# Performance work log

Measured on AMD Instinct MI355X. Metric: run time of the kernel, lower is better.

The kernel has to match this reference:

```python
import jax, jax.numpy as jnp
import numpy as np
from jax import lax

DIM = 128
HEADS = 2
SR = 4
HID = 512  # 4 * DIM
DROPKEY_P = 0.1


def _ln(x, g, b, eps=1e-5):
    m = jnp.mean(x, axis=-1, keepdims=True)
    v = jnp.var(x, axis=-1, keepdims=True)
    return (x - m) / jnp.sqrt(v + eps) * g + b


def _block(x, H, W, params, key):
    (n1g, n1b, qw, kvw, srw, srb, sng, snb, pw, pb,
     n2g, n2b, f1w, f1b, dww, dwb, f2w, f2b) = params
    B, N, C = x.shape
    dh = C // HEADS
    scale = dh ** -0.5
    # --- spatial-reduction attention ---
    h = _ln(x, n1g, n1b)
    q = (h @ qw.T).reshape(B, N, HEADS, dh).transpose(0, 2, 1, 3)  # [B,h,N,dh]
    xi = h.transpose(0, 2, 1).reshape(B, C, H, W)
    xs = lax.conv_general_dilated(xi, srw, (SR, SR), 'VALID',
                                  dimension_numbers=('NCHW', 'OIHW', 'NCHW'))
    xs = xs + srb[None, :, None, None]
    Np = (H // SR) * (W // SR)
    xs = xs.reshape(B, C, Np).transpose(0, 2, 1)  # [B,N',C]
    xs = _ln(xs, sng, snb)
    kv = (xs @ kvw.T).reshape(B, Np, 2, HEADS, dh).transpose(2, 0, 3, 1, 4)
    k, v = kv[0], kv[1]  # [B,h,N',dh]
    attn = jnp.einsum('bhnd,bhmd->bhnm', q, k) * scale
    # dropkey: bernoulli(p) mask pushed to -1e12 before softmax (always applied)
    mask = jax.random.bernoulli(key, DROPKEY_P, attn.shape)
    attn = attn + mask.astype(attn.dtype) * (-1e12)
    attn = jax.nn.softmax(attn, axis=-1)
    o = jnp.einsum('bhnm,bhmd->bhnd', attn, v).transpose(0, 2, 1, 3).reshape(B, N, C)
    x = x + o @ pw.T + pb
    # --- MLP with depthwise conv ---
    h2 = _ln(x, n2g, n2b)
    h2 = h2 @ f1w.T + f1b  # [B,N,HID]
    hi = h2.transpose(0, 2, 1).reshape(B, HID, H, W)
    hi = lax.conv_general_dilated(hi, dww, (1, 1), 'SAME',
                                  feature_group_count=HID,
                                  dimension_numbers=('NCHW', 'OIHW', 'NCHW'))
    hi = hi + dwb[None, :, None, None]
    h2 = hi.reshape(B, HID, N).transpose(0, 2, 1)
    h2 = jax.nn.gelu(h2, approximate=False)
    x = x + h2 @ f2w.T + f2b
    return x


def setup_inputs() -> dict:
    key = jax.random.key(0)
    ks = jax.random.split(key, 10)
    p = {}
    p['x'] = jax.random.normal(ks[0], (16, 2 * DIM, 56, 56), jnp.float32)
    p['concat_w'] = jax.random.normal(ks[1], (DIM, 2 * DIM), jnp.float32) * 0.02
    p['concat_b'] = jnp.zeros((DIM,), jnp.float32)
    # two Blocks -> leading dim 2 on all per-block params
    p['norm1_g'] = jnp.ones((2, DIM), jnp.float32)
    p['norm1_b'] = jnp.zeros((2, DIM), jnp.float32)
    p['q_w'] = jax.random.normal(ks[2], (2, DIM, DIM), jnp.float32) * 0.02
    p['kv_w'] = jax.random.normal(ks[3], (2, 2 * DIM, DIM), jnp.float32) * 0.02
    p['sr_w'] = jax.random.normal(ks[4], (2, DIM, DIM, SR, SR), jnp.float32) * 0.03
    p['sr_b'] = jnp.zeros((2, DIM), jnp.float32)
    p['srn_g'] = jnp.ones((2, DIM), jnp.float32)
    p['srn_b'] = jnp.zeros((2, DIM), jnp.float32)
    p['proj_w'] = jax.random.normal(ks[5], (2, DIM, DIM), jnp.float32) * 0.02
    p['proj_b'] = jnp.zeros((2, DIM), jnp.float32)
    p['norm2_g'] = jnp.ones((2, DIM), jnp.float32)
    p['norm2_b'] = jnp.zeros((2, DIM), jnp.float32)
    p['fc1_w'] = jax.random.normal(ks[6], (2, HID, DIM), jnp.float32) * 0.02
    p['fc1_b'] = jnp.zeros((2, HID), jnp.float32)
    p['dw_w'] = jax.random.normal(ks[7], (2, HID, 1, 3, 3), jnp.float32) * 0.1
    p['dw_b'] = jnp.zeros((2, HID), jnp.float32)
    p['fc2_w'] = jax.random.normal(ks[8], (2, DIM, HID), jnp.float32) * 0.02
    p['fc2_b'] = jnp.zeros((2, DIM), jnp.float32)
    return p


def reference(x, concat_w, concat_b, norm1_g, norm1_b, q_w, kv_w, sr_w, sr_b,
              srn_g, srn_b, proj_w, proj_b, norm2_g, norm2_b, fc1_w, fc1_b,
              dw_w, dw_b, fc2_w, fc2_b):
    b, c, h, w = x.shape
    xs = x.transpose(0, 2, 3, 1).reshape(b, h * w, c)
    xs = xs @ concat_w.T + concat_b  # [B,N,DIM]
    mkey = jax.random.key(42)
    stacked = (norm1_g, norm1_b, q_w, kv_w, sr_w, sr_b, srn_g, srn_b, proj_w,
               proj_b, norm2_g, norm2_b, fc1_w, fc1_b, dw_w, dw_b, fc2_w, fc2_b)
    for i in range(2):
        params_i = tuple(p[i] for p in stacked)
        xs = _block(xs, h, w, params_i, jax.random.fold_in(mkey, i))
    return xs.reshape(b, h, w, DIM).transpose(0, 3, 1, 2)
```

## Files before the change

### kernel.cpp

```cpp
#include <hip/hip_runtime.h>
#include <stdint.h>

typedef __attribute__((ext_vector_type(8))) short short8;
typedef __attribute__((ext_vector_type(4))) float f32x4;
typedef __attribute__((ext_vector_type(2))) float f32x2;
typedef unsigned short u16;
typedef uint32_t u32;
typedef unsigned long long u64;

__host__ __device__ static inline void threefry(u32 k0, u32 k1, u32 x0, u32 x1,
                                                u32* o0, u32* o1) {
  u32 ks2 = k0 ^ k1 ^ 0x1BD11BDAu;
  x0 += k0; x1 += k1;
#define TF_RR(r) { x0 += x1; x1 = (x1 << (r)) | (x1 >> (32 - (r))); x1 ^= x0; }
  TF_RR(13) TF_RR(15) TF_RR(26) TF_RR(6)
  x0 += k1;  x1 += ks2 + 1u;
  TF_RR(17) TF_RR(29) TF_RR(16) TF_RR(24)
  x0 += ks2; x1 += k0 + 2u;
  TF_RR(13) TF_RR(15) TF_RR(26) TF_RR(6)
  x0 += k0;  x1 += k1 + 3u;
  TF_RR(17) TF_RR(29) TF_RR(16) TF_RR(24)
  x0 += k1;  x1 += ks2 + 4u;
  TF_RR(13) TF_RR(15) TF_RR(26) TF_RR(6)
  x0 += ks2; x1 += k0 + 5u;
#undef TF_RR
  *o0 = x0; *o1 = x1;
}

__device__ static inline float bf2f(u16 u) {
  union { u32 i; float f; } v; v.i = ((u32)u) << 16; return v.f;
}
__device__ static inline u16 f2bf(float f) {
  union { float f; u32 i; } v; v.f = f;
  u32 x = v.i;
  return (u16)((x + 0x7FFFu + ((x >> 16) & 1u)) >> 16);
}
__device__ static inline float lo_bf(u32 w) {
  union { u32 i; float f; } v; v.i = w << 16; return v.f;
}
__device__ static inline float hi_bf(u32 w) {
  union { u32 i; float f; } v; v.i = w & 0xFFFF0000u; return v.f;
}
__device__ static inline bool is_f32(const u32* ng) { return ng[0] == 0x3F800000u; }

typedef const uint32_t __attribute__((address_space(1)))* gas_ptr;
typedef uint32_t __attribute__((address_space(3)))* las_ptr;
__device__ static inline void gld16(const u16* g, u16* l) {
  __builtin_amdgcn_global_load_lds((gas_ptr)(const void*)g, (las_ptr)(void*)l, 16, 0, 0);
}

#define MASK_HALF 9834496u

__global__ __launch_bounds__(256) void mask_gen2(u32* __restrict__ MSK2, u32 k0, u32 k1) {
  int t = blockIdx.x * 256 + threadIdx.x;
  if (t >= 351232) return;
  int w = t % 7;
  int rowbh = t / 7;
  u32 base = (u32)rowbh * 196u + (u32)w * 32u;
  int kmax = 196 - w * 32;
  if (kmax > 32) kmax = 32;
  u32 bits0 = 0, bits1 = 0;
  for (int j = 0; j < kmax; j++) {
    u32 o0, o1;
    threefry(k0, k1, base + (u32)j, base + (u32)j + MASK_HALF, &o0, &o1);
    union { u32 u; float f; } u0, u1;
    u0.u = (o0 >> 9) | 0x3F800000u;
    u1.u = (o1 >> 9) | 0x3F800000u;
    if (u0.f - 1.0f < 0.1f) bits0 |= (1u << j);
    if (u1.f - 1.0f < 0.1f) bits1 |= (1u << j);
  }
  MSK2[(size_t)rowbh * 7 + w] = bits0;
  MSK2[(size_t)(rowbh + 50176) * 7 + w] = bits1;
}

struct PtrTab { const void* p[20]; };
#define ARENA_N 963968
#define VT_WORDS 229376

__global__ __launch_bounds__(256) void convert_params(PtrTab tab, u16* __restrict__ arena,
                                                      u32* __restrict__ VT) {
  const int cum[21] = {0, 32768, 32896, 33152, 33408, 66176, 131712, 656000, 656256,
                       656512, 656768, 689536, 689792, 690048, 690304, 821376, 822400,
                       831616, 832640, 963712, 963968};
  int idx = blockIdx.x * 256 + threadIdx.x;
  if (idx >= ARENA_N) {
    int v = idx - ARENA_N;
    if (v < VT_WORDS) VT[v] = 0;
    return;
  }
  bool f32m = (((const u32*)tab.p[2])[0] == 0x3F800000u);
  int t = 0;
  while (idx >= cum[t + 1]) t++;
  int local = idx - cum[t];
  if (t == 16) {
    int blk = local / 4608, r = local - blk * 4608;
    int wi = r >> 9, c = r & 511;
    local = blk * 4608 + c * 9 + wi;
  } else if (t == 6) {
    int blk = local / 262144, r = local - blk * 262144;
    int o = r >> 11, kp = r & 2047;
    int ij = kp >> 7, c = kp & 127;
    local = blk * 262144 + o * 2048 + c * 16 + ij;
  }
  u16 v;
  if (f32m) v = f2bf(((const float*)tab.p[t])[local]);
  else      v = ((const u16*)tab.p[t])[local];
  arena[idx] = v;
}

__global__ __launch_bounds__(256) void transpose_in(const void* __restrict__ Xin,
                                                    const u32* __restrict__ ng,
                                                    u16* __restrict__ Xt) {
  bool f32m = is_f32(ng);
  __shared__ u16 tile[64][65];
  int n0 = blockIdx.x * 64, c0 = blockIdx.y * 64, b = blockIdx.z;
  int tx = threadIdx.x & 63, ty = threadIdx.x >> 6;
  if (f32m) {
    const float* src = (const float*)Xin + (size_t)b * 256 * 3136;
#pragma unroll
    for (int i = 0; i < 16; i++) {
      int cl = i * 4 + ty;
      tile[cl][tx] = f2bf(src[(size_t)(c0 + cl) * 3136 + n0 + tx]);
    }
  } else {
    const u16* src = (const u16*)Xin + (size_t)b * 256 * 3136;
#pragma unroll
    for (int i = 0; i < 16; i++) {
      int cl = i * 4 + ty;
      tile[cl][tx] = src[(size_t)(c0 + cl) * 3136 + n0 + tx];
    }
  }
  __syncthreads();
  u16* dst = Xt + (size_t)b * 3136 * 256;
#pragma unroll
  for (int i = 0; i < 16; i++) {
    int nl = i * 4 + ty;
    dst[(size_t)(n0 + nl) * 256 + c0 + tx] = tile[tx][nl];
  }
}

__global__ __launch_bounds__(256) void transpose_out(const u16* __restrict__ X,
                                                     const u32* __restrict__ ng,
                                                     void* __restrict__ Out) {
  bool f32m = is_f32(ng);
  __shared__ u16 tile[64][65];
  int n0 = blockIdx.x * 64, d0 = blockIdx.y * 64, b = blockIdx.z;
  int tx = threadIdx.x & 63, ty = threadIdx.x >> 6;
#pragma unroll
  for (int i = 0; i < 16; i++) {
    int nl = i * 4 + ty;
    tile[nl][tx] = X[((size_t)b * 3136 + n0 + nl) * 128 + d0 + tx];
  }
  __syncthreads();
#pragma unroll
  for (int i = 0; i < 16; i++) {
    int dl = i * 4 + ty;
    size_t o = ((size_t)b * 128 + d0 + dl) * 3136 + n0 + tx;
    if (f32m) ((float*)Out)[o] = bf2f(tile[tx][dl]);
    else      ((u16*)Out)[o]   = tile[tx][dl];
  }
}

__global__ __launch_bounds__(256) __attribute__((amdgpu_waves_per_eu(2, 4)))
void gemm_tiled(const u16* __restrict__ A,
                const u16* __restrict__ W,
                const u16* __restrict__ bias,
                u16* __restrict__ outB,
                u16* __restrict__ outVT,
                int M, int N, int K, int mode) {
  __shared__ __align__(16) u16 smem[17408];
  u16* AlsP = smem;
  u16* BlsP = smem + 8192;
  int n0 = blockIdx.y * 128, m0 = blockIdx.x * 128;
  int tid = threadIdx.x, wv = tid >> 6, lane = tid & 63;
  int wr = wv >> 1, wc = wv & 1;
  int l15 = lane & 15, hh = lane >> 4, lk = hh * 8;
  int srow = wv * 32 + (lane >> 2);
  int scol = (lane & 3) * 8;

  f32x4 acc[4][4];
#pragma unroll
  for (int m = 0; m < 4; m++)
#pragma unroll
    for (int n = 0; n < 4; n++) acc[m][n] = (f32x4){0.f, 0.f, 0.f, 0.f};

#define STAGE(buf, k0)                                                          \
  {                                                                             \
    _Pragma("unroll") for (int i = 0; i < 2; i++) {                             \
      int ar = m0 + srow + i * 16;                                              \
      if (ar >= M) ar = M - 1;                                                  \
      gld16(A + (size_t)ar * K + (k0) + scol,                                   \
            AlsP + (buf) * 4096 + (wv * 32 + i * 16) * 32);                     \
      int br = n0 + srow + i * 16;                                              \
      gld16(W + (size_t)br * K + (k0) + scol,                                   \
            BlsP + (buf) * 4096 + (wv * 32 + i * 16) * 32);                     \
    }                                                                           \
  }

  int nt = K >> 5;
  STAGE(0, 0);
  int cur = 0;
  for (int t = 0; t < nt; t++) {
    __syncthreads();
    if (t + 1 < nt) STAGE(cur ^ 1, (t + 1) * 32);
    short8 af[4], bf[4];
#pragma unroll
    for (int m = 0; m < 4; m++)
      af[m] = *(const short8*)(AlsP + cur * 4096 + (wr * 64 + m * 16 + l15) * 32 + lk);
#pragma unroll
    for (int n = 0; n < 4; n++)
      bf[n] = *(const short8*)(BlsP + cur * 4096 + (wc * 64 + n * 16 + l15) * 32 + lk);
#pragma unroll
    for (int m = 0; m < 4; m++)
#pragma unroll
      for (int n = 0; n < 4; n++)
        acc[m][n] = __builtin_amdgcn_mfma_f32_16x16x32_bf16(af[m], bf[n], acc[m][n], 0, 0, 0);
    cur ^= 1;
  }
#undef STAGE

  if (mode == 0) {
    __syncthreads();
#pragma unroll
    for (int n = 0; n < 4; n++) {
      int col = wc * 64 + n * 16 + l15;
      float bv = bias ? bf2f(bias[n0 + col]) : 0.0f;
#pragma unroll
      for (int m = 0; m < 4; m++) {
        int rbase = wr * 64 + m * 16 + hh * 4;
#pragma unroll
        for (int r = 0; r < 4; r++)
          smem[(rbase + r) * 136 + col] = f2bf(acc[m][n][r] + bv);
      }
    }
    __syncthreads();
#pragma unroll
    for (int p = 0; p < 8; p++) {
      int row = p * 16 + (tid >> 4);
      int colb = (tid & 15) * 8;
      int grow = m0 + row;
      if (grow < M) {
        short8 v = *(const short8*)&smem[row * 136 + colb];
        *(short8*)(outB + (size_t)grow * N + n0 + colb) = v;
      }
    }
    return;
  }

#pragma unroll
  for (int n = 0; n < 4; n++) {
    int col = n0 + wc * 64 + n * 16 + l15;
#pragma unroll
    for (int m = 0; m < 4; m++) {
      int rbase = m0 + wr * 64 + m * 16 + hh * 4;
#pragma unroll
      for (int r = 0; r < 4; r++) {
        int row = rbase + r;
        if (row < M) {
          float v = acc[m][n][r];
          if (col < 128) outB[(size_t)row * 128 + col] = f2bf(v);
          else {
            int hd = (col - 128) >> 6, d = (col - 128) & 63;
            int b = row / 196, key = row - b * 196;
            outVT[(size_t)((b * 2 + hd) * 64 + d) * 224 + key] = f2bf(v);
          }
        }
      }
    }
  }
}

__global__ __launch_bounds__(256) __attribute__((amdgpu_waves_per_eu(2, 4)))
void gemm_n128(const u16* __restrict__ A,
               const u16* __restrict__ W,
               const u16* __restrict__ bias,
               u16* __restrict__ Xb,
               u16* __restrict__ outB,
               const u16* __restrict__ lnG,
               const u16* __restrict__ lnB,
               u16* __restrict__ outH,
               const u16* __restrict__ qW,
               u16* __restrict__ outQ,
               int M, int K, int mode) {
  __shared__ __align__(16) u16 smem[12288];
  __shared__ float sumsA[64][4];
  __shared__ float sumsB[64][4];
  u16* Als = smem;
  u16* Bls = smem + 4096;
  int m0 = blockIdx.y * 64;
  int tid = threadIdx.x, wv = tid >> 6, lane = tid & 63;
  int l15 = lane & 15, hq = lane >> 4, lk = hq * 8;
  int scol = (lane & 3) * 8;

  f32x4 acc[4][2];
#pragma unroll
  for (int m = 0; m < 4; m++)
#pragma unroll
    for (int n = 0; n < 2; n++) acc[m][n] = (f32x4){0.f, 0.f, 0.f, 0.f};

#define STAGE(buf, k0)                                                          \
  {                                                                             \
    int ar = m0 + wv * 16 + (lane >> 2);                                        \
    if (ar >= M) ar = M - 1;                                                    \
    gld16(A + (size_t)ar * K + (k0) + scol, Als + (buf) * 2048 + wv * 512);     \
    _Pragma("unroll") for (int i = 0; i < 2; i++) {                             \
      int br = wv * 32 + i * 16 + (lane >> 2);                                  \
      gld16(W + (size_t)br * K + (k0) + scol,                                   \
            Bls + (buf) * 4096 + wv * 1024 + i * 512);                          \
    }                                                                           \
  }

  int nt = K >> 5;
  STAGE(0, 0);
  int cur = 0;
  for (int t = 0; t < nt; t++) {
    __syncthreads();
    if (t + 1 < nt) STAGE(cur ^ 1, (t + 1) * 32);
    short8 af[4], bf[2];
#pragma unroll
    for (int m = 0; m < 4; m++)
      af[m] = *(const short8*)(Als + cur * 2048 + (m * 16 + l15) * 32 + lk);
#pragma unroll
    for (int n = 0; n < 2; n++)
      bf[n] = *(const short8*)(Bls + cur * 4096 + (wv * 32 + n * 16 + l15) * 32 + lk);
#pragma unroll
    for (int m = 0; m < 4; m++)
#pragma unroll
      for (int n = 0; n < 2; n++)
        acc[m][n] = __builtin_amdgcn_mfma_f32_16x16x32_bf16(af[m], bf[n], acc[m][n], 0, 0, 0);
    cur ^= 1;
  }
#undef STAGE

  if (mode == 2) {
#pragma unroll
    for (int n = 0; n < 2; n++) {
      int col = wv * 32 + n * 16 + l15;
      float bv = bias ? bf2f(bias[col]) : 0.0f;
#pragma unroll
      for (int m = 0; m < 4; m++) {
        int rbase = m0 + m * 16 + hq * 4;
#pragma unroll
        for (int r = 0; r < 4; r++) {
          size_t idx = (size_t)(rbase + r) * 128 + col;
          Xb[idx] = f2bf(bf2f(Xb[idx]) + acc[m][n][r] + bv);
        }
      }
    }
    return;
  }

  if (mode >= 4) {
#pragma unroll
    for (int n = 0; n < 2; n++) {
      int col = wv * 32 + n * 16 + l15;
      float bv = bias ? bf2f(bias[col]) : 0.0f;
#pragma unroll
      for (int m = 0; m < 4; m++) {
        int rbase = m0 + m * 16 + hq * 4;
#pragma unroll
        for (int r = 0; r < 4; r++) {
          size_t idx = (size_t)(rbase + r) * 128 + col;
          float v = acc[m][n][r] + bv;
          if (mode == 5) v += bf2f(Xb[idx]);
          acc[m][n][r] = v;
          Xb[idx] = f2bf(v);
        }
      }
    }
#pragma unroll
    for (int m = 0; m < 4; m++) {
#pragma unroll
      for (int r = 0; r < 4; r++) {
        float a = acc[m][0][r] + acc[m][1][r];
        float b = acc[m][0][r] * acc[m][0][r] + acc[m][1][r] * acc[m][1][r];
#pragma unroll
        for (int d = 1; d < 16; d <<= 1) {
          a += __shfl_xor(a, d);
          b += __shfl_xor(b, d);
        }
        if (l15 == 0) {
          int lrow = m * 16 + hq * 4 + r;
          sumsA[lrow][wv] = a;
          sumsB[lrow][wv] = b;
        }
      }
    }
    __syncthreads();
#pragma unroll
    for (int m = 0; m < 4; m++) {
#pragma unroll
      for (int r = 0; r < 4; r++) {
        int lrow = m * 16 + hq * 4 + r;
        float t1 = sumsA[lrow][0] + sumsA[lrow][1] + sumsA[lrow][2] + sumsA[lrow][3];
        float t2 = sumsB[lrow][0] + sumsB[lrow][1] + sumsB[lrow][2] + sumsB[lrow][3];
        float mean = t1 * 0.0078125f;
        float var = t2 * 0.0078125f - mean * mean;
        float inv = 1.0f / sqrtf(var + 1e-5f);
#pragma unroll
        for (int n = 0; n < 2; n++) {
          int col = wv * 32 + n * 16 + l15;
          float g = bf2f(lnG[col]), bb2 = bf2f(lnB[col]);
          smem[lrow * 136 + col] = f2bf((acc[m][n][r] - mean) * inv * g + bb2);
        }
      }
    }
    __syncthreads();
#pragma unroll
    for (int p = 0; p < 4; p++) {
      int row = p * 16 + (tid >> 4);
      int colb = (tid & 15) * 8;
      short8 v = *(const short8*)&smem[row * 136 + colb];
      *(short8*)(outH + (size_t)(m0 + row) * 128 + colb) = v;
    }

    if (qW) {
#pragma unroll
      for (int m = 0; m < 4; m++)
#pragma unroll
        for (int n = 0; n < 2; n++) acc[m][n] = (f32x4){0.f, 0.f, 0.f, 0.f};
#pragma unroll
      for (int kc = 0; kc < 4; kc++) {
        short8 af[4], bf[2];
#pragma unroll
        for (int m = 0; m < 4; m++)
          af[m] = *(const short8*)&smem[(m * 16 + l15) * 136 + kc * 32 + lk];
#pragma unroll
        for (int n = 0; n < 2; n++)
          bf[n] = *(const short8*)(qW + (size_t)(wv * 32 + n * 16 + l15) * 128 +
                                   kc * 32 + lk);
#pragma unroll
        for (int m = 0; m < 4; m++)
#pragma unroll
          for (int n = 0; n < 2; n++)
            acc[m][n] =
                __builtin_amdgcn_mfma_f32_16x16x32_bf16(af[m], bf[n], acc[m][n], 0, 0, 0);
      }
      __syncthreads();
#pragma unroll
      for (int n = 0; n < 2; n++) {
        int col = wv * 32 + n * 16 + l15;
#pragma unroll
        for (int m = 0; m < 4; m++) {
          int rbase = m * 16 + hq * 4;
#pragma unroll
          for (int r = 0; r < 4; r++)
            smem[(rbase + r) * 136 + col] = f2bf(acc[m][n][r]);
        }
      }
      __syncthreads();
#pragma unroll
      for (int p = 0; p < 4; p++) {
        int row = p * 16 + (tid >> 4);
        int colb = (tid & 15) * 8;
        short8 v = *(const short8*)&smem[row * 136 + colb];
        *(short8*)(outQ + (size_t)(m0 + row) * 128 + colb) = v;
      }
    }
    return;
  }

  __syncthreads();
#pragma unroll
  for (int n = 0; n < 2; n++) {
    int col = wv * 32 + n * 16 + l15;
    float bv = bias ? bf2f(bias[col]) : 0.0f;
#pragma unroll
    for (int m = 0; m < 4; m++) {
      int rbase = m * 16 + hq * 4;
#pragma unroll
      for (int r = 0; r < 4; r++)
        smem[(rbase + r) * 136 + col] = f2bf(acc[m][n][r] + bv);
    }
  }
  __syncthreads();
#pragma unroll
  for (int p = 0; p < 4; p++) {
    int row = p * 16 + (tid >> 4);
    int colb = (tid & 15) * 8;
    short8 v = *(const short8*)&smem[row * 136 + colb];
    *(short8*)(outB + (size_t)(m0 + row) * 128 + colb) = v;
  }
}

__global__ __launch_bounds__(256) void gemm_splitk(const u16* __restrict__ Hsrc,
                                                   const u16* __restrict__ W,
                                                   float* __restrict__ PS,
                                                   int M, int N, int K) {
  __shared__ __align__(16) u16 Als[2][4096];
  __shared__ __align__(16) u16 Bls[2][4096];
  int n0 = blockIdx.x * 128, m0 = blockIdx.y * 128, ks = blockIdx.z;
  int tid = threadIdx.x, wv = tid >> 6, lane = tid & 63;
  int wr = wv >> 1, wc = wv & 1;
  int l15 = lane & 15, lk = (lane >> 4) * 8;
  int srow = wv * 32 + (lane >> 2);
  int scol = (lane & 3) * 8;

  f32x4 acc[4][4];
#pragma unroll
  for (int m = 0; m < 4; m++)
#pragma unroll
    for (int n = 0; n < 4; n++) acc[m][n] = (f32x4){0.f, 0.f, 0.f, 0.f};

#define STAGE(buf, k0)                                                          \
  {                                                                             \
    _Pragma("unroll") for (int i = 0; i < 2; i++) {                             \
      int ar = m0 + srow + i * 16;                                              \
      if (ar >= M) ar = M - 1;                                                  \
      int bb = ar / 196, pp = ar - bb * 196;                                    \
      int ph = pp / 14, pw = pp - ph * 14;                                      \
      int kk = (k0) + scol;                                                     \
      int ij = kk >> 7, c = kk & 127;                                           \
      int n2 = (4 * ph + (ij >> 2)) * 56 + 4 * pw + (ij & 3);                   \
      gld16(Hsrc + ((size_t)(bb * 3136 + n2)) * 128 + c,                        \
            &Als[buf][(wv * 32 + i * 16) * 32]);                                \
      int br = n0 + srow + i * 16;                                              \
      gld16(W + (size_t)br * K + (k0) + scol,                                   \
            &Bls[buf][(wv * 32 + i * 16) * 32]);                                \
    }                                                                           \
  }

  int kbeg = ks * 128;
  STAGE(0, kbeg);
  int cur = 0;
  for (int t = 0; t < 4; t++) {
    __syncthreads();
    if (t + 1 < 4) STAGE(cur ^ 1, kbeg + (t + 1) * 32);
    short8 af[4], bf[4];
#pragma unroll
    for (int m = 0; m < 4; m++)
      af[m] = *(const short8*)(&Als[cur][(wr * 64 + m * 16 + l15) * 32 + lk]);
#pragma unroll
    for (int n = 0; n < 4; n++)
      bf[n] = *(const short8*)(&Bls[cur][(wc * 64 + n * 16 + l15) * 32 + lk]);
#pragma unroll
    for (int m = 0; m < 4; m++)
#pragma unroll
      for (int n = 0; n < 4; n++)
        acc[m][n] = __builtin_amdgcn_mfma_f32_16x16x32_bf16(af[m], bf[n], acc[m][n], 0, 0, 0);
    cur ^= 1;
  }
#undef STAGE

  float* myPS = PS + (size_t)ks * M * N;
#pragma unroll
  for (int n = 0; n < 4; n++) {
    int col = n0 + wc * 64 + n * 16 + l15;
#pragma unroll
    for (int m = 0; m < 4; m++) {
      int rbase = m0 + wr * 64 + m * 16 + (lane >> 4) * 4;
#pragma unroll
      for (int r = 0; r < 4; r++) {
        int row = rbase + r;
        if (row < M) myPS[(size_t)row * N + col] = acc[m][n][r];
      }
    }
  }
}

__global__ __launch_bounds__(256) void splitk_reduce_ln(const float* __restrict__ PS,
                                                        const u16* __restrict__ bias,
                                                        const u16* __restrict__ G,
                                                        const u16* __restrict__ Bi,
                                                        u16* __restrict__ XSN) {
  __shared__ float red[4][2];
  int tid = threadIdx.x;
  int row = blockIdx.x * 2 + (tid >> 7);
  int col = tid & 127;
  int t = row * 128 + col;
  float s = bf2f(bias[col]);
#pragma unroll
  for (int k = 0; k < 16; k++) s += PS[(size_t)k * 401408 + t];
  float s1 = s, s2 = s * s;
#pragma unroll
  for (int d = 1; d < 64; d <<= 1) {
    s1 += __shfl_xor(s1, d);
    s2 += __shfl_xor(s2, d);
  }
  int wv = tid >> 6;
  if ((tid & 63) == 0) { red[wv][0] = s1; red[wv][1] = s2; }
  __syncthreads();
  int other = wv ^ 1;
  float t1 = red[wv][0] + red[other][0];
  float t2 = red[wv][1] + red[other][1];
  float mean = t1 * 0.0078125f;
  float var = t2 * 0.0078125f - mean * mean;
  float inv = 1.0f / sqrtf(var + 1e-5f);
  XSN[t] = f2bf((s - mean) * inv * bf2f(G[col]) + bf2f(Bi[col]));
}

__global__ __launch_bounds__(256) __attribute__((amdgpu_waves_per_eu(2, 4)))
void attn_kernel(const u16* __restrict__ Q,
                 const u16* __restrict__ Kb,
                 const u16* __restrict__ VT,
                 const u32* __restrict__ M2,
                 u16* __restrict__ O) {
  __shared__ __align__(16) u16 smA[14848];
  int t = blockIdx.x;
  int tp = (t & 7) * 196 + (t >> 3);
  int bh = tp / 49, qt = tp - bh * 49;
  int b = bh >> 1, hd = bh & 1;
  int q0 = qt * 64;
  int tid = threadIdx.x;

  int wv = tid >> 6, lane = tid & 63;
  int l15 = lane & 15, h = lane >> 4, lk = h * 8;

  {
    const u16* ksrc = Kb + (size_t)b * 196 * 128 + hd * 64;
    for (int idx = tid; idx < 1568; idx += 256) {
      int row = idx >> 3, ch = idx & 7;
      short8 v = *(const short8*)(ksrc + (size_t)row * 128 + ch * 8);
      *(short8*)&smA[row * 68 + ch * 8] = v;
    }
  }

  const u16* qp = Q + ((size_t)(b * 3136 + q0 + wv * 16 + l15) * 128) + hd * 64 + lk;
  short8 aq0 = *(const short8*)(qp);
  short8 aq1 = *(const short8*)(qp + 32);
  int rowg = q0 + wv * 16 + h * 4;

  u32 mwv[4][7];
  const u32* mwbase = M2 + (size_t)(bh * 3136 + rowg) * 7;
#pragma unroll
  for (int r = 0; r < 4; r++)
#pragma unroll
    for (int w = 0; w < 7; w++) mwv[r][w] = mwbase[r * 7 + w];

  __syncthreads();

  float sarr[13][4];
#pragma unroll
  for (int cc = 0; cc < 13; cc++) {
    int key = cc * 16 + l15;
    int keyc = key > 195 ? 195 : key;
    short8 kb0 = *(const short8*)&smA[keyc * 68 + lk];
    short8 kb1 = *(const short8*)&smA[keyc * 68 + 32 + lk];
    f32x4 s = {0.f, 0.f, 0.f, 0.f};
    s = __builtin_amdgcn_mfma_f32_16x16x32_bf16(aq0, kb0, s, 0, 0, 0);
    s = __builtin_amdgcn_mfma_f32_16x16x32_bf16(aq1, kb1, s, 0, 0, 0);
#pragma unroll
    for (int r = 0; r < 4; r++) sarr[cc][r] = s[r] * 0.125f;
  }

#pragma unroll
  for (int cc = 0; cc < 13; cc++) {
    bool keyok = (cc * 16 + l15) < 196;
    int pos = (cc & 3) * 16 + l15;
#pragma unroll
    for (int r = 0; r < 4; r++) {
      u64 mm = (cc < 4) ? ((u64)mwv[r][0] | ((u64)mwv[r][1] << 32))
             : (cc < 8) ? ((u64)mwv[r][2] | ((u64)mwv[r][3] << 32))
             : (cc < 12) ? ((u64)mwv[r][4] | ((u64)mwv[r][5] << 32))
                         : ((u64)mwv[r][6]);
      bool drop = (mm >> pos) & 1ull;
      if (!keyok || drop) sarr[cc][r] = -3.0e38f;
    }
  }

  float mx[4] = {sarr[0][0], sarr[0][1], sarr[0][2], sarr[0][3]};
#pragma unroll
  for (int cc = 1; cc < 13; cc++)
#pragma unroll
    for (int r = 0; r < 4; r++) mx[r] = fmaxf(mx[r], sarr[cc][r]);
#pragma unroll
  for (int d = 1; d < 16; d <<= 1)
#pragma unroll
    for (int r = 0; r < 4; r++) mx[r] = fmaxf(mx[r], __shfl_xor(mx[r], d));
  float sm[4] = {0.f, 0.f, 0.f, 0.f};
#pragma unroll
  for (int cc = 0; cc < 13; cc++)
#pragma unroll
    for (int r = 0; r < 4; r++) {
      float p = __expf(sarr[cc][r] - mx[r]);
      sarr[cc][r] = p;
      sm[r] += p;
    }
#pragma unroll
  for (int d = 1; d < 16; d <<= 1)
#pragma unroll
    for (int r = 0; r < 4; r++) sm[r] += __shfl_xor(sm[r], d);
  float inv[4];
#pragma unroll
  for (int r = 0; r < 4; r++)
    asm("v_rcp_f32 %0, %1" : "=v"(inv[r]) : "v"(sm[r]));

  __syncthreads();

#pragma unroll
  for (int cc = 0; cc < 13; cc++)
#pragma unroll
    for (int r = 0; r < 4; r++)
      smA[(wv * 16 + h * 4 + r) * 232 + cc * 16 + l15] = f2bf(sarr[cc][r] * inv[r]);
#pragma unroll
  for (int rj = 0; rj < 4; rj++) smA[(wv * 16 + l15) * 232 + 208 + h * 4 + rj] = 0;

  const u16* vbase = VT + (size_t)(bh * 64) * 224;
  short8 vw[4];
#pragma unroll
  for (int i = 0; i < 4; i++) {
    vw[i] = *(const short8*)(vbase + (size_t)(0 * 16 + l15) * 224 + i * 32 + lk);
  }
#pragma unroll
  for (int dc = 0; dc < 4; dc++) {
    f32x4 oa = {0.f, 0.f, 0.f, 0.f};
#pragma unroll
    for (int kc = 0; kc < 7; kc++) {
      int i = dc * 7 + kc;
      short8 bv = vw[i & 3];
      if (i + 4 < 28) {
        int i2 = i + 4;
        int dc2 = i2 / 7, kc2 = i2 - dc2 * 7;
        vw[i & 3] =
            *(const short8*)(vbase + (size_t)(dc2 * 16 + l15) * 224 + kc2 * 32 + lk);
      }
      short8 a = *(const short8*)&smA[(wv * 16 + l15) * 232 + kc * 32 + lk];
      oa = __builtin_amdgcn_mfma_f32_16x16x32_bf16(a, bv, oa, 0, 0, 0);
    }
#pragma unroll
    for (int r = 0; r < 4; r++) {
      O[((size_t)(b * 3136 + rowg + r) * 128) + hd * 64 + dc * 16 + l15] = f2bf(oa[r]);
    }
  }
}

__global__ __launch_bounds__(256) __attribute__((amdgpu_waves_per_eu(2, 4)))
void dwconv_gelu(const u16* __restrict__ H2,
                 const u16* __restrict__ Wdw,
                 const u16* __restrict__ Bdw,
                 u16* __restrict__ Out) {
  int tid = threadIdx.x;
  int wv = tid >> 6, lane = tid & 63;
  int sb = blockIdx.x;
  int wg = (sb & 7) * 392 + (sb >> 3);
  int strip = wg * 4 + wv;
  int bb = strip / 784;
  int s = strip - bb * 784;
  int y = s / 14, x0 = (s - y * 14) * 4;
  int c0 = lane * 8;

  f32x2 wf[9][4];
#pragma unroll
  for (int t9 = 0; t9 < 9; t9++) {
    short8 w8 = *(const short8*)(Wdw + t9 * 512 + c0);
#pragma unroll
    for (int p = 0; p < 4; p++) {
      u32 w = ((const u32*)&w8)[p];
      wf[t9][p] = (f32x2){lo_bf(w), hi_bf(w)};
    }
  }
  f32x2 acc[4][4];
  {
    short8 b8 = *(const short8*)(Bdw + c0);
#pragma unroll
    for (int p = 0; p < 4; p++) {
      u32 w = ((const u32*)&b8)[p];
      f32x2 bv = {lo_bf(w), hi_bf(w)};
#pragma unroll
      for (int q = 0; q < 4; q++) acc[q][p] = bv;
    }
  }

  const u16* base = H2 + ((size_t)bb * 3136) * 512 + c0;
#pragma unroll
  for (int di = -1; di <= 1; di++) {
    int y2 = y + di;
    if (y2 < 0 || y2 >= 56) continue;
    const u16* rowp = base + (size_t)(y2 * 56) * 512;
#pragma unroll
    for (int j = 0; j < 6; j++) {
      int c = x0 - 1 + j;
      if (c < 0 || c > 55) continue;
      short8 h8 = *(const short8*)(rowp + (size_t)c * 512);
      f32x2 hf[4];
#pragma unroll
      for (int p = 0; p < 4; p++) {
        u32 w = ((const u32*)&h8)[p];
        hf[p] = (f32x2){lo_bf(w), hi_bf(w)};
      }
      int wrow = (di + 1) * 3;
#pragma unroll
      for (int q = 0; q < 4; q++) {
        int dx = j - 1 - q;
        if (dx < -1 || dx > 1) continue;
#pragma unroll
        for (int p = 0; p < 4; p++) acc[q][p] += hf[p] * wf[wrow + dx + 1][p];
      }
    }
  }

  size_t obase = ((size_t)(bb * 3136 + y * 56 + x0)) * 512 + c0;
#pragma unroll
  for (int q = 0; q < 4; q++) {
    short8 ov;
#pragma unroll
    for (int p = 0; p < 4; p++) {
      float g2[2];
#pragma unroll
      for (int e = 0; e < 2; e++) {
        float v = acc[q][p][e];
        float tt = v * v;
        float yn = v * (-2.3022088f - 0.1029434f * tt);
        float ex;
        asm("v_exp_f32 %0, %1" : "=v"(ex) : "v"(yn));
        float den = 1.0f + ex;
        float sg;
        asm("v_rcp_f32 %0, %1" : "=v"(sg) : "v"(den));
        g2[e] = v * sg;
      }
      u32 pk;
      asm("v_cvt_pk_bf16_f32 %0, %1, %2" : "=v"(pk) : "v"(g2[0]), "v"(g2[1]));
      ((u32*)&ov)[p] = pk;
    }
    *(short8*)(Out + obase + (size_t)q * 512) = ov;
  }
}

__global__ __launch_bounds__(256) void fill_sentinel(void* __restrict__ Out,
                                                     const u32* __restrict__ ng, int n) {
  bool f32m = is_f32(ng);
  int t = blockIdx.x * 256 + threadIdx.x;
  if (t >= n) return;
  if (f32m) ((float*)Out)[t] = 12345.0f;
  else      ((u16*)Out)[t]   = f2bf(12345.0f);
}

extern "C" void kernel_launch(void* const* d_in, const int* in_sizes, int n_in,
                              void* d_out, int out_size, void* d_ws, size_t ws_size,
                              hipStream_t stream) {
  (void)in_sizes; (void)n_in;
  const u32* ng = (const u32*)d_in[3];

  const size_t o_X   = 0;
  const size_t o_H   = 25690112;
  const size_t o_R   = o_H + 12845056;
  const size_t o_Q   = o_R;
  const size_t o_O   = o_R + 12845056;
  const size_t o_Xt  = o_R + 25690112;
  const size_t o_H2C = o_R;
  const size_t o_H2  = o_R + 51380224;
  const size_t o_XSN = o_H2 + 51380224;
  const size_t o_KB  = o_XSN + 802816;
  const size_t o_VT  = o_KB + 802816;
  const size_t o_M2  = o_VT + 917504;
  const size_t o_AR  = o_M2 + 2809856;
  const size_t NEED  = o_AR + (size_t)ARENA_N * 2;

  if (ws_size < NEED) {
    fill_sentinel<<<(out_size + 255) / 256, 256, 0, stream>>>(d_out, ng, out_size);
    return;
  }

  char* ws = (char*)d_ws;
  u16* Xb   = (u16*)(ws + o_X);
  u16* H    = (u16*)(ws + o_H);
  u16* Qb   = (u16*)(ws + o_Q);
  u16* Ob   = (u16*)(ws + o_O);
  u16* Xt   = (u16*)(ws + o_Xt);
  u16* H2C  = (u16*)(ws + o_H2C);
  u16* H2   = (u16*)(ws + o_H2);
  float* PS = (float*)(ws + o_H2);
  u16* XSN  = (u16*)(ws + o_XSN);
  u16* Kb   = (u16*)(ws + o_KB);
  u16* VT   = (u16*)(ws + o_VT);
  u32* MSK2 = (u32*)(ws + o_M2);
  u16* AR   = (u16*)(ws + o_AR);

  PtrTab tab;
  for (int j = 0; j < 20; j++) tab.p[j] = d_in[j + 1];
  convert_params<<<(ARENA_N + VT_WORDS + 255) / 256, 256, 0, stream>>>(tab, AR, (u32*)VT);

  u16* ACW  = AR + 0;      u16* ACB  = AR + 32768;
  u16* AN1G = AR + 32896;  u16* AN1B = AR + 33152;
  u16* AQW  = AR + 33408;  u16* AKVW = AR + 66176;
  u16* ASRW = AR + 131712; u16* ASRB = AR + 656000;
  u16* ASNG = AR + 656256; u16* ASNB = AR + 656512;
  u16* APW  = AR + 656768; u16* APB  = AR + 689536;
  u16* AN2G = AR + 689792; u16* AN2B = AR + 690048;
  u16* AF1W = AR + 690304; u16* AF1B = AR + 821376;
  u16* ADWW = AR + 822400; u16* ADWB = AR + 831616;
  u16* AF2W = AR + 832640; u16* AF2B = AR + 963712;

  transpose_in<<<dim3(49, 4, 16), 256, 0, stream>>>(d_in[0], ng, Xt);
  gemm_n128<<<dim3(1, 784), 256, 0, stream>>>(Xt, ACW, ACB, Xb, nullptr,
                                              AN1G, AN1B, H, AQW, Qb,
                                              50176, 256, 4);

  for (int i = 0; i < 2; i++) {
    u32 fk0, fk1;
    threefry(0u, 42u, 0u, (u32)i, &fk0, &fk1);

    gemm_splitk<<<dim3(1, 25, 16), 256, 0, stream>>>(H, ASRW + i * 262144, PS,
                                                     3136, 128, 2048);
    mask_gen2<<<1372, 256, 0, stream>>>(MSK2, fk0, fk1);
    splitk_reduce_ln<<<1568, 256, 0, stream>>>(PS, ASRB + i * 128,
                                               ASNG + i * 128, ASNB + i * 128, XSN);

    gemm_tiled<<<dim3(25, 2), 256, 0, stream>>>(XSN, AKVW + i * 32768, nullptr,
                                                Kb, VT, 3136, 256, 128, 3);
    attn_kernel<<<1568, 256, 0, stream>>>(Qb, Kb, VT, MSK2, Ob);
    gemm_n128<<<dim3(1, 784), 256, 0, stream>>>(Ob, APW + i * 16384, APB + i * 128,
                                                Xb, nullptr,
                                                AN2G + i * 128, AN2B + i * 128, H,
                                                nullptr, nullptr, 50176, 128, 5);
    gemm_tiled<<<dim3(392, 4), 256, 0, stream>>>(H, AF1W + i * 65536, AF1B + i * 512,
                                                 H2, nullptr,
                                                 50176, 512, 128, 0);
    dwconv_gelu<<<3136, 256, 0, stream>>>(H2, ADWW + i * 4608, ADWB + i * 512, H2C);
    if (i == 0) {
      gemm_n128<<<dim3(1, 784), 256, 0, stream>>>(H2C, AF2W, AF2B, Xb, nullptr,
                                                  AN1G + 128, AN1B + 128, H,
                                                  AQW + 16384, Qb, 50176, 512, 5);
    } else {
      gemm_n128<<<dim3(1, 784), 256, 0, stream>>>(H2C, AF2W + 65536, AF2B + 128,
                                                  Xb, nullptr, nullptr, nullptr, nullptr,
                                                  nullptr, nullptr, 50176, 512, 2);
    }
  }

  transpose_out<<<dim3(49, 2, 16), 256, 0, stream>>>(Xb, ng, d_out);
}
```

Before: 410.0 us.

## Restructure gemm_n128 so each wave owns 16 full rows, dropping LDS staging

Each wave now computes a 16x128 output tile, with A and W fragments loaded straight from global memory instead of being staged through double-buffered shared memory. LayerNorm row statistics are then reduced with shuffles inside the wave, so the cross-wave shared-memory sums and the block barriers go away. The fused Q projection also runs per wave on the wave's own LDS slice. In exchange W is re-read from global/L2 by every wave with no LDS reuse, the mode<4 plain-output path (outB) is removed, and the M bounds clamp is dropped.

```diff
diff --git a/kernel.cpp b/kernel.cpp
--- a/kernel.cpp
+++ b/kernel.cpp
@@ -282,204 +282,115 @@
                const u16* __restrict__ qW,
                u16* __restrict__ outQ,
                int M, int K, int mode) {
-  __shared__ __align__(16) u16 smem[12288];
-  __shared__ float sumsA[64][4];
-  __shared__ float sumsB[64][4];
-  u16* Als = smem;
-  u16* Bls = smem + 4096;
-  int m0 = blockIdx.y * 64;
+  (void)outB; (void)M;
+  __shared__ __align__(16) u16 smem[8704];
   int tid = threadIdx.x, wv = tid >> 6, lane = tid & 63;
-  int l15 = lane & 15, hq = lane >> 4, lk = hq * 8;
-  int scol = (lane & 3) * 8;
-
-  f32x4 acc[4][2];
-#pragma unroll
-  for (int m = 0; m < 4; m++)
-#pragma unroll
-    for (int n = 0; n < 2; n++) acc[m][n] = (f32x4){0.f, 0.f, 0.f, 0.f};
-
-#define STAGE(buf, k0)                                                          \
-  {                                                                             \
-    int ar = m0 + wv * 16 + (lane >> 2);                                        \
-    if (ar >= M) ar = M - 1;                                                    \
-    gld16(A + (size_t)ar * K + (k0) + scol, Als + (buf) * 2048 + wv * 512);     \
-    _Pragma("unroll") for (int i = 0; i < 2; i++) {                             \
-      int br = wv * 32 + i * 16 + (lane >> 2);                                  \
-      gld16(W + (size_t)br * K + (k0) + scol,                                   \
-            Bls + (buf) * 4096 + wv * 1024 + i * 512);                          \
-    }                                                                           \
-  }
-
+  int l15 = lane & 15, h = lane >> 4, lk = h * 8;
+  int mw = blockIdx.y * 64 + wv * 16;
+  u16* ws = smem + wv * 2176;
+
+  f32x4 acc[8];
+#pragma unroll
+  for (int n = 0; n < 8; n++) acc[n] = (f32x4){0.f, 0.f, 0.f, 0.f};
+
+  const u16* arow = A + (size_t)(mw + l15) * K + lk;
   int nt = K >> 5;
-  STAGE(0, 0);
-  int cur = 0;
   for (int t = 0; t < nt; t++) {
-    __syncthreads();
-    if (t + 1 < nt) STAGE(cur ^ 1, (t + 1) * 32);
-    short8 af[4], bf[2];
-#pragma unroll
-    for (int m = 0; m < 4; m++)
-      af[m] = *(const short8*)(Als + cur * 2048 + (m * 16 + l15) * 32 + lk);
-#pragma unroll
-    for (int n = 0; n < 2; n++)
-      bf[n] = *(const short8*)(Bls + cur * 4096 + (wv * 32 + n * 16 + l15) * 32 + lk);
-#pragma unroll
-    for (int m = 0; m < 4; m++)
-#pragma unroll
-      for (int n = 0; n < 2; n++)
-        acc[m][n] = __builtin_amdgcn_mfma_f32_16x16x32_bf16(af[m], bf[n], acc[m][n], 0, 0, 0);
-    cur ^= 1;
-  }
-#undef STAGE
+    short8 af = *(const short8*)(arow + t * 32);
+    short8 bf[8];
+#pragma unroll
+    for (int n = 0; n < 8; n++)
+      bf[n] = *(const short8*)(W + (size_t)(n * 16 + l15) * K + t * 32 + lk);
+#pragma unroll
+    for (int n = 0; n < 8; n++)
+      acc[n] = __builtin_amdgcn_mfma_f32_16x16x32_bf16(af, bf[n], acc[n], 0, 0, 0);
+  }
 
   if (mode == 2) {
 #pragma unroll
-    for (int n = 0; n < 2; n++) {
-      int col = wv * 32 + n * 16 + l15;
+    for (int n = 0; n < 8; n++) {
+      int col = n * 16 + l15;
       float bv = bias ? bf2f(bias[col]) : 0.0f;
 #pragma unroll
-      for (int m = 0; m < 4; m++) {
-        int rbase = m0 + m * 16 + hq * 4;
-#pragma unroll
-        for (int r = 0; r < 4; r++) {
-          size_t idx = (size_t)(rbase + r) * 128 + col;
-          Xb[idx] = f2bf(bf2f(Xb[idx]) + acc[m][n][r] + bv);
-        }
+      for (int r = 0; r < 4; r++) {
+        size_t idx = (size_t)(mw + h * 4 + r) * 128 + col;
+        Xb[idx] = f2bf(bf2f(Xb[idx]) + acc[n][r] + bv);
       }
     }
     return;
   }
 
-  if (mode >= 4) {
-#pragma unroll
-    for (int n = 0; n < 2; n++) {
-      int col = wv * 32 + n * 16 + l15;
-      float bv = bias ? bf2f(bias[col]) : 0.0f;
-#pragma unroll
-      for (int m = 0; m < 4; m++) {
-        int rbase = m0 + m * 16 + hq * 4;
-#pragma unroll
-        for (int r = 0; r < 4; r++) {
-          size_t idx = (size_t)(rbase + r) * 128 + col;
-          float v = acc[m][n][r] + bv;
-          if (mode == 5) v += bf2f(Xb[idx]);
-          acc[m][n][r] = v;
-          Xb[idx] = f2bf(v);
-        }
-      }
-    }
-#pragma unroll
-    for (int m = 0; m < 4; m++) {
-#pragma unroll
-      for (int r = 0; r < 4; r++) {
-        float a = acc[m][0][r] + acc[m][1][r];
-        float b = acc[m][0][r] * acc[m][0][r] + acc[m][1][r] * acc[m][1][r];
-#pragma unroll
-        for (int d = 1; d < 16; d <<= 1) {
-          a += __shfl_xor(a, d);
-          b += __shfl_xor(b, d);
-        }
-        if (l15 == 0) {
-          int lrow = m * 16 + hq * 4 + r;
-          sumsA[lrow][wv] = a;
-          sumsB[lrow][wv] = b;
-        }
-      }
-    }
-    __syncthreads();
-#pragma unroll
-    for (int m = 0; m < 4; m++) {
-#pragma unroll
-      for (int r = 0; r < 4; r++) {
-        int lrow = m * 16 + hq * 4 + r;
-        float t1 = sumsA[lrow][0] + sumsA[lrow][1] + sumsA[lrow][2] + sumsA[lrow][3];
-        float t2 = sumsB[lrow][0] + sumsB[lrow][1] + sumsB[lrow][2] + sumsB[lrow][3];
-        float mean = t1 * 0.0078125f;
-        float var = t2 * 0.0078125f - mean * mean;
-        float inv = 1.0f / sqrtf(var + 1e-5f);
-#pragma unroll
-        for (int n = 0; n < 2; n++) {
-          int col = wv * 32 + n * 16 + l15;
-          float g = bf2f(lnG[col]), bb2 = bf2f(lnB[col]);
-          smem[lrow * 136 + col] = f2bf((acc[m][n][r] - mean) * inv * g + bb2);
-        }
-      }
-    }
-    __syncthreads();
+#pragma unroll
+  for (int n = 0; n < 8; n++) {
+    int col = n * 16 + l15;
+    float bv = bias ? bf2f(bias[col]) : 0.0f;
+#pragma unroll
+    for (int r = 0; r < 4; r++) {
+      size_t idx = (size_t)(mw + h * 4 + r) * 128 + col;
+      float v = acc[n][r] + bv;
+      if (mode == 5) v += bf2f(Xb[idx]);
+      acc[n][r] = v;
+      Xb[idx] = f2bf(v);
+    }
+  }
+#pragma unroll
+  for (int r = 0; r < 4; r++) {
+    float a = 0.f, b = 0.f;
+#pragma unroll
+    for (int n = 0; n < 8; n++) {
+      a += acc[n][r];
+      b += acc[n][r] * acc[n][r];
+    }
+#pragma unroll
+    for (int d = 1; d < 16; d <<= 1) {
+      a += __shfl_xor(a, d);
+      b += __shfl_xor(b, d);
+    }
+    float mean = a * 0.0078125f;
+    float var = b * 0.0078125f - mean * mean;
+    float inv = 1.0f / sqrtf(var + 1e-5f);
+#pragma unroll
+    for (int n = 0; n < 8; n++) {
+      int col = n * 16 + l15;
+      ws[(h * 4 + r) * 136 + col] =
+          f2bf((acc[n][r] - mean) * inv * bf2f(lnG[col]) + bf2f(lnB[col]));
+    }
+  }
+#pragma unroll
+  for (int p = 0; p < 4; p++) {
+    int row = p * 4 + h;
+    int colb = l15 * 8;
+    short8 v = *(const short8*)&ws[row * 136 + colb];
+    *(short8*)(outH + (size_t)(mw + row) * 128 + colb) = v;
+  }
+
+  if (qW) {
+    f32x4 qa[8];
+#pragma unroll
+    for (int n = 0; n < 8; n++) qa[n] = (f32x4){0.f, 0.f, 0.f, 0.f};
+#pragma unroll
+    for (int kc = 0; kc < 4; kc++) {
+      short8 aq = *(const short8*)&ws[l15 * 136 + kc * 32 + lk];
+      short8 bq[8];
+#pragma unroll
+      for (int n = 0; n < 8; n++)
+        bq[n] = *(const short8*)(qW + (size_t)(n * 16 + l15) * 128 + kc * 32 + lk);
+#pragma unroll
+      for (int n = 0; n < 8; n++)
+        qa[n] = __builtin_amdgcn_mfma_f32_16x16x32_bf16(aq, bq[n], qa[n], 0, 0, 0);
+    }
+#pragma unroll
+    for (int n = 0; n < 8; n++)
+#pragma unroll
+      for (int r = 0; r < 4; r++)
+        ws[(h * 4 + r) * 136 + n * 16 + l15] = f2bf(qa[n][r]);
 #pragma unroll
     for (int p = 0; p < 4; p++) {
-      int row = p * 16 + (tid >> 4);
-      int colb = (tid & 15) * 8;
-      short8 v = *(const short8*)&smem[row * 136 + colb];
-      *(short8*)(outH + (size_t)(m0 + row) * 128 + colb) = v;
-    }
-
-    if (qW) {
-#pragma unroll
-      for (int m = 0; m < 4; m++)
-#pragma unroll
-        for (int n = 0; n < 2; n++) acc[m][n] = (f32x4){0.f, 0.f, 0.f, 0.f};
-#pragma unroll
-      for (int kc = 0; kc < 4; kc++) {
-        short8 af[4], bf[2];
-#pragma unroll
-        for (int m = 0; m < 4; m++)
-          af[m] = *(const short8*)&smem[(m * 16 + l15) * 136 + kc * 32 + lk];
-#pragma unroll
-        for (int n = 0; n < 2; n++)
-          bf[n] = *(const short8*)(qW + (size_t)(wv * 32 + n * 16 + l15) * 128 +
-                                   kc * 32 + lk);
-#pragma unroll
-        for (int m = 0; m < 4; m++)
-#pragma unroll
-          for (int n = 0; n < 2; n++)
-            acc[m][n] =
-                __builtin_amdgcn_mfma_f32_16x16x32_bf16(af[m], bf[n], acc[m][n], 0, 0, 0);
-      }
-      __syncthreads();
-#pragma unroll
-      for (int n = 0; n < 2; n++) {
-        int col = wv * 32 + n * 16 + l15;
-#pragma unroll
-        for (int m = 0; m < 4; m++) {
-          int rbase = m * 16 + hq * 4;
-#pragma unroll
-          for (int r = 0; r < 4; r++)
-            smem[(rbase + r) * 136 + col] = f2bf(acc[m][n][r]);
-        }
-      }
-      __syncthreads();
-#pragma unroll
-      for (int p = 0; p < 4; p++) {
-        int row = p * 16 + (tid >> 4);
-        int colb = (tid & 15) * 8;
-        short8 v = *(const short8*)&smem[row * 136 + colb];
-        *(short8*)(outQ + (size_t)(m0 + row) * 128 + colb) = v;
-      }
-    }
-    return;
-  }
-
-  __syncthreads();
-#pragma unroll
-  for (int n = 0; n < 2; n++) {
-    int col = wv * 32 + n * 16 + l15;
-    float bv = bias ? bf2f(bias[col]) : 0.0f;
-#pragma unroll
-    for (int m = 0; m < 4; m++) {
-      int rbase = m * 16 + hq * 4;
-#pragma unroll
-      for (int r = 0; r < 4; r++)
-        smem[(rbase + r) * 136 + col] = f2bf(acc[m][n][r] + bv);
-    }
-  }
-  __syncthreads();
-#pragma unroll
-  for (int p = 0; p < 4; p++) {
-    int row = p * 16 + (tid >> 4);
-    int colb = (tid & 15) * 8;
-    short8 v = *(const short8*)&smem[row * 136 + colb];
-    *(short8*)(outB + (size_t)(m0 + row) * 128 + colb) = v;
+      int row = p * 4 + h;
+      int colb = l15 * 8;
+      short8 v = *(const short8*)&ws[row * 136 + colb];
+      *(short8*)(outQ + (size_t)(mw + row) * 128 + colb) = v;
+    }
   }
 }
 
```

New measurement: 557.5 us. 1.36x slower.
